# Kernel optimization log

Measured on AMD Instinct MI355X. Metric: run time of the kernel, lower is better.

Reference implementation:

```python
import jax, jax.numpy as jnp
import numpy as np

B, T, C, N = 4, 12, 64, 10000
H = 64            # d_inner (GRU hidden)
L = 2             # num_layers
NE = 2000         # number of static hyperedges
NNZ = 80000       # incidence list length
TOPK = 10         # HGCNADP_topk
DE = 16           # HGCNADP_embed_dims
RATE = 0.5        # hyperedge_rate (blend static vs adaptive)


def setup_inputs() -> dict:
    key = jax.random.key(0)
    ks = jax.random.split(key, 10)
    scale = 0.05
    x = jax.random.normal(ks[0], (B, T, C, N), jnp.float32)
    node_idx = jax.random.randint(ks[1], (NNZ,), 0, N, jnp.int32)
    edge_idx = jax.random.randint(ks[2], (NNZ,), 0, NE, jnp.int32)
    hyperedge_index = jnp.stack([node_idx, edge_idx])  # (2, NNZ)
    node_embs = jax.random.normal(ks[3], (L, N, DE), jnp.float32) * 0.1
    W_zr = jax.random.normal(ks[4], (L, C + H, 2 * H), jnp.float32) * scale
    b_zr = jnp.zeros((L, 2 * H), jnp.float32)
    W_c = jax.random.normal(ks[5], (L, C + H, H), jnp.float32) * scale
    b_c = jnp.zeros((L, H), jnp.float32)
    W_out = jax.random.normal(ks[6], (L, H, C), jnp.float32) * scale
    b_out = jnp.zeros((L, C), jnp.float32)
    return {"x": x, "hyperedge_index": hyperedge_index, "node_embs": node_embs,
            "W_zr": W_zr, "b_zr": b_zr, "W_c": W_c, "b_c": b_c,
            "W_out": W_out, "b_out": b_out}


def reference(x, hyperedge_index, node_embs, W_zr, b_zr, W_c, b_c, W_out, b_out):
    # x: (B, T, C, N). Dropout is identity (eval mode).
    node_idx = hyperedge_index[0]
    edge_idx = hyperedge_index[1]
    edge_deg = jnp.zeros((NE,), x.dtype).at[edge_idx].add(1.0)
    inv_e = 1.0 / jnp.maximum(edge_deg, 1.0)
    node_deg = jnp.zeros((N,), x.dtype).at[node_idx].add(1.0)
    inv_n = 1.0 / jnp.maximum(node_deg, 1.0)

    def conv(f, topk_idx, topk_w):
        # f: (B, N, D). Static hypergraph pass: node -> hyperedge -> node.
        msg = jnp.take(f, node_idx, axis=1)                       # (B, NNZ, D)
        eagg = jnp.zeros((f.shape[0], NE, f.shape[2]), f.dtype).at[:, edge_idx].add(msg)
        eagg = eagg * inv_e[None, :, None]                        # (B, NE, D)
        stat = jnp.zeros_like(f).at[:, node_idx].add(jnp.take(eagg, edge_idx, axis=1))
        stat = stat * inv_n[None, :, None]                        # (B, N, D)
        # Adaptive top-k hyperedge aggregation (softmax-weighted neighbor sum).
        adp = jnp.einsum('bnkd,nk->bnd', jnp.take(f, topk_idx, axis=1), topk_w)
        return RATE * stat + (1.0 - RATE) * adp

    out = x
    for l in range(L):
        xl = out.transpose(0, 1, 3, 2)                            # (B, T, N, C)
        E = node_embs[l]
        scores = jax.nn.relu(E @ E.T)                             # (N, N)
        vals, idx = jax.lax.top_k(scores, TOPK)                   # (N, K)
        w = jax.nn.softmax(vals, axis=-1)
        Wz, bz = W_zr[l], b_zr[l]
        Wc_, bc_ = W_c[l], b_c[l]
        Wo, bo = W_out[l], b_out[l]

        def step(h, x_t):
            zr = jax.nn.sigmoid(conv(jnp.concatenate([x_t, h], -1), idx, w) @ Wz + bz)
            z, r = jnp.split(zr, 2, axis=-1)
            c = jnp.tanh(conv(jnp.concatenate([x_t, r * h], -1), idx, w) @ Wc_ + bc_)
            h_new = z * h + (1.0 - z) * c
            return h_new, h_new @ Wo + bo

        h0 = jnp.zeros((out.shape[0], N, H), x.dtype)
        _, ys = jax.lax.scan(step, h0, xl.transpose(1, 0, 2, 3))  # ys: (T, B, N, C)
        out = out + ys.transpose(1, 0, 3, 2)                      # residual, back to (B,T,C,N)
    return out
```

## Files before the change

### kernel.cpp

```cpp
#include <hip/hip_runtime.h>
#include <hip/hip_fp16.h>
#include <cstdio>

#define BB 4
#define TT 12
#define CC 64
#define NN 10000
#define HH 64
#define LL 2
#define NEDGE 2000
#define NNZT 80000
#define KTOP 10
#define DEMB 16
#define BT (BB*TT)
#define TOPK_BLKS 1250
#define TRN_BLKS 30048
#define NB16 625

typedef long long ll;
typedef unsigned long long u64;
typedef unsigned int u32;
typedef unsigned short ushort;

typedef short bf16x8 __attribute__((ext_vector_type(8)));
typedef float f32x4 __attribute__((ext_vector_type(4)));

__device__ __forceinline__ void up8(const uint4 v, float* f) {
  const __half2* p = reinterpret_cast<const __half2*>(&v);
  float2 t0 = __half22float2(p[0]);
  float2 t1 = __half22float2(p[1]);
  float2 t2 = __half22float2(p[2]);
  float2 t3 = __half22float2(p[3]);
  f[0]=t0.x; f[1]=t0.y; f[2]=t1.x; f[3]=t1.y;
  f[4]=t2.x; f[5]=t2.y; f[6]=t3.x; f[7]=t3.y;
}
__device__ __forceinline__ uint4 pk8(const float* f) {
  __half2 h0 = __floats2half2_rn(f[0], f[1]);
  __half2 h1 = __floats2half2_rn(f[2], f[3]);
  __half2 h2 = __floats2half2_rn(f[4], f[5]);
  __half2 h3 = __floats2half2_rn(f[6], f[7]);
  uint4 r;
  r.x = *reinterpret_cast<unsigned*>(&h0);
  r.y = *reinterpret_cast<unsigned*>(&h1);
  r.z = *reinterpret_cast<unsigned*>(&h2);
  r.w = *reinterpret_cast<unsigned*>(&h3);
  return r;
}
__device__ __forceinline__ ushort f2bf(float x) {
  u32 u = __float_as_uint(x);
  u32 r = u + 0x7FFFu + ((u >> 16) & 1u);
  return (ushort)(r >> 16);
}
__device__ __forceinline__ uint4 pk8bf(const float* f) {
  uint4 r;
  r.x = (u32)f2bf(f[0]) | ((u32)f2bf(f[1])<<16);
  r.y = (u32)f2bf(f[2]) | ((u32)f2bf(f[3])<<16);
  r.z = (u32)f2bf(f[4]) | ((u32)f2bf(f[5])<<16);
  r.w = (u32)f2bf(f[6]) | ((u32)f2bf(f[7])<<16);
  return r;
}

__global__ void deg_kernel(const int* __restrict__ nidx, const int* __restrict__ eidx,
                           int* __restrict__ ndeg, int* __restrict__ edeg) {
  int i = blockIdx.x*256 + threadIdx.x;
  if (i < NNZT) { atomicAdd(&ndeg[nidx[i]],1); atomicAdd(&edeg[eidx[i]],1); }
}

__global__ void exscan_kernel(const int* __restrict__ cnt, int* __restrict__ off, int n) {
  __shared__ int part[256];
  int tid = threadIdx.x;
  int chunk = (n + 255)/256;
  int lo = tid*chunk, hi = min(lo+chunk, n);
  int s = 0;
  for (int i=lo; i<hi; ++i) s += cnt[i];
  part[tid]=s; __syncthreads();
  if (tid==0){ int acc=0; for(int i=0;i<256;++i){int v=part[i];part[i]=acc;acc+=v;} off[n]=acc; }
  __syncthreads();
  int acc = part[tid];
  for (int i=lo; i<hi; ++i){ off[i]=acc; acc+=cnt[i]; }
}

__global__ void fill_csr_kernel(const int* __restrict__ nidx, const int* __restrict__ eidx,
                                const int* __restrict__ noff, const int* __restrict__ eoff,
                                int* __restrict__ ncur, int* __restrict__ ecur,
                                int* __restrict__ node_edges, int* __restrict__ edge_nodes) {
  int i = blockIdx.x*256 + threadIdx.x;
  if (i >= NNZT) return;
  int n = nidx[i], e = eidx[i];
  int pn = atomicAdd(&ncur[n],1);
  node_edges[noff[n]+pn] = e;
  int pe = atomicAdd(&ecur[e],1);
  edge_nodes[eoff[e]+pe] = n;
}

__global__ void invdeg_kernel(const int* __restrict__ ndeg, const int* __restrict__ edeg,
                              float* __restrict__ inv_n, float* __restrict__ inv_e) {
  int i = blockIdx.x*256+threadIdx.x;
  if (i < NN) inv_n[i] = 1.0f/fmaxf((float)ndeg[i],1.0f);
  if (i < NEDGE) inv_e[i] = 1.0f/fmaxf((float)edeg[i],1.0f);
}

__global__ void prep_w_kernel(const float* __restrict__ W_zr, const float* __restrict__ W_c,
                              const float* __restrict__ W_o,
                              short* __restrict__ Wz_swb, short* __restrict__ Wc_swb,
                              short* __restrict__ Wo_swb) {
  int l = blockIdx.y;
  const float* Wz = W_zr + (size_t)l*128*128;
  const float* Wc = W_c  + (size_t)l*128*64;
  const float* Wo = W_o  + (size_t)l*64*64;
  short* Wz_sw = Wz_swb + (size_t)l*16384;
  short* Wc_sw = Wc_swb + (size_t)l*8192;
  short* Wo_sw = Wo_swb + (size_t)l*4096;
  int idx = blockIdx.x*256 + threadIdx.x;
  if (idx < 16384) {
    int i = idx&7, lane = (idx>>3)&63, kk = (idx>>9)&3, tc = idx>>11;
    int k = kk*32 + (lane>>4)*8 + i, col = tc*16 + (lane&15);
    Wz_sw[idx] = (short)f2bf(Wz[k*128+col]);
  }
  if (idx < 8192) {
    int i = idx&7, lane = (idx>>3)&63, kk = (idx>>9)&3, tc = idx>>11;
    int k = kk*32 + (lane>>4)*8 + i, col = tc*16 + (lane&15);
    Wc_sw[idx] = (short)f2bf(Wc[k*64+col]);
  }
  if (idx < 4096) {
    int i = idx&7, lane = (idx>>3)&63, kk = (idx>>9)&1, tc = idx>>10;
    int k = kk*32 + (lane>>4)*8 + i, col = tc*16 + (lane&15);
    Wo_sw[idx] = (short)f2bf(Wo[k*64+col]);
  }
}

__device__ __forceinline__ u64 sortstep(u64 X, int j, bool dir, int lane) {
  u64 p = __shfl_xor(X, j);
  bool lower = ((lane & j) == 0);
  bool keep_min = (dir == lower);
  bool xlt = (X < p);
  u64 mn = xlt ? X : p;
  u64 mx = xlt ? p : X;
  return keep_min ? mn : mx;
}

__device__ __forceinline__ void reselect(u64* bq, u64& thr, int& cnt, int lane) {
  int tot = 10 + cnt;
  u64 A = (lane < tot)      ? bq[lane]      : 0ull;
  u64 B = (lane + 64 < tot) ? bq[lane + 64] : 0ull;
  for (int k = 2; k <= 32; k <<= 1) {
    for (int j = k >> 1; j >= 1; j >>= 1) {
      bool dir = ((lane & k) == 0);
      A = sortstep(A, j, dir, lane);
      B = sortstep(B, j, dir, lane);
    }
  }
  for (int j = 32; j >= 1; j >>= 1) {
    A = sortstep(A, j, true,  lane);
    B = sortstep(B, j, false, lane);
  }
  {
    bool lt = (A < B);
    u64 mn = lt ? A : B, mx = lt ? B : A;
    A = mn; B = mx;
  }
  for (int j = 32; j >= 1; j >>= 1) {
    A = sortstep(A, j, true, lane);
    B = sortstep(B, j, true, lane);
  }
  if (lane >= 54) bq[63 - lane] = B;
  thr = __shfl(B, 54);
  cnt = 0;
}

__device__ void topk_body(int layer, int qb, char* smem,
                          const float* __restrict__ embs, int2* __restrict__ tkc_b) {
  u64 (*buf)[128] = (u64(*)[128])smem;
  const float* E = embs + (ll)layer*NN*DEMB;
  int2* tkc = tkc_b + (ll)layer*NN*KTOP;
  int tid = threadIdx.x;
  int wv = tid >> 6, lane = tid & 63;
  int qbase = qb*16 + wv*4;
  const float4* E4 = (const float4*)E;
  float4 q[4][4];
  #pragma unroll
  for (int u=0;u<4;++u) {
    int n = qbase + u;
    #pragma unroll
    for (int j=0;j<4;++j) q[u][j] = E4[(ll)n*4 + j];
  }
  u64 thr[4] = {0,0,0,0};
  float thrf[4] = {0.f,0.f,0.f,0.f};
  int cnt[4] = {0,0,0,0};
  buf[tid>>4][tid&15] = 0ull;
  float4 a0,a1,a2,a3;
  {
    int ca = (lane < NN) ? lane : 0;
    a0=E4[(ll)ca*4]; a1=E4[(ll)ca*4+1]; a2=E4[(ll)ca*4+2]; a3=E4[(ll)ca*4+3];
  }
  for (int cb=0; cb<NN; cb+=64) {
    float4 b0,b1,b2,b3;
    int ncb = cb + 64;
    if (ncb < NN) {
      int cand2 = ncb + lane;
      int ca2 = (cand2 < NN) ? cand2 : 0;
      b0=E4[(ll)ca2*4]; b1=E4[(ll)ca2*4+1]; b2=E4[(ll)ca2*4+2]; b3=E4[(ll)ca2*4+3];
    }
    int cand = cb + lane;
    bool valid = (cand < NN);
    u64 low = (u64)(0x00FFFFFFu - (unsigned)cand);
    float sv[4];
    #pragma unroll
    for (int u=0;u<4;++u) {
      float dot = q[u][0].x*a0.x + q[u][0].y*a0.y + q[u][0].z*a0.z + q[u][0].w*a0.w
                + q[u][1].x*a1.x + q[u][1].y*a1.y + q[u][1].z*a1.z + q[u][1].w*a1.w
                + q[u][2].x*a2.x + q[u][2].y*a2.y + q[u][2].z*a2.z + q[u][2].w*a2.w
                + q[u][3].x*a3.x + q[u][3].y*a3.y + q[u][3].z*a3.z + q[u][3].w*a3.w;
      float s = fmaxf(dot, 0.f);
      sv[u] = valid ? s : -1.f;
    }
    bool hitany = (sv[0]>=thrf[0]) | (sv[1]>=thrf[1]) | (sv[2]>=thrf[2]) | (sv[3]>=thrf[3]);
    u64 anym = __ballot(hitany);
    if (anym) {
      #pragma unroll
      for (int u=0;u<4;++u) {
        u64 mask = __ballot(sv[u] >= thrf[u]);
        if (mask) {
          if (sv[u] >= thrf[u]) {
            u64 key = ((u64)__float_as_uint(sv[u]) << 32) | low;
            int myofs = (int)__popcll(mask & ((1ull<<lane)-1ull));
            buf[wv*4+u][10 + cnt[u] + myofs] = key;
          }
          cnt[u] += (int)__popcll(mask);
          if (cnt[u] >= 40) {
            reselect(&buf[wv*4+u][0], thr[u], cnt[u], lane);
            thrf[u] = __uint_as_float((u32)(thr[u] >> 32));
          }
        }
      }
    }
    a0=b0; a1=b1; a2=b2; a3=b3;
  }
  #pragma unroll
  for (int u=0;u<4;++u) {
    u64* bq = &buf[wv*4+u][0];
    if (cnt[u] > 0) reselect(bq, thr[u], cnt[u], lane);
    u64 k10 = (lane < 10) ? bq[lane] : 0ull;
    float v = __uint_as_float((unsigned)(k10 >> 32));
    int idx = 0x00FFFFFF - (int)(k10 & 0xFFFFFFFFull);
    float v0 = __shfl(v, 0);
    float e = (lane < 10) ? expf(v - v0) : 0.f;
    float s = e;
    for (int o=1;o<16;o<<=1) s += __shfl_xor(s, o);
    if (lane < 10) {
      int n = qbase + u;
      tkc[n*KTOP + lane] = make_int2(idx, __float_as_int(e / s));
    }
  }
}

__device__ void transpose_body(int tb, char* smem,
                               const float* __restrict__ src, __half* __restrict__ dst) {
  float (*tile)[33] = (float(*)[33])smem;
  int tid = threadIdx.x;
  int tx = tid & 31, ty = tid >> 5;
  int bt = tb / 626;
  int rem = tb % 626;
  int n0 = (rem % 313)*32, c0 = (rem/313)*32;
  for (int i=ty; i<32; i+=8) {
    int c = c0+i, nn = n0+tx;
    tile[i][tx] = (nn<NN)? src[((ll)bt*CC + c)*NN + nn] : 0.0f;
  }
  __syncthreads();
  for (int i=ty; i<32; i+=8) {
    int nn = n0+i, c = c0+tx;
    if (nn<NN) dst[((ll)bt*NN+nn)*64 + c] = __float2half_rn(tile[tx][i]);
  }
}

__global__ void __launch_bounds__(256) mega1_kernel(const float* __restrict__ embs,
                                                    int2* __restrict__ tkc,
                                                    const float* __restrict__ x,
                                                    __half* __restrict__ xt) {
  __shared__ __align__(16) char smem[16384];
  int bid = blockIdx.x;
  if (bid < TOPK_BLKS) topk_body(bid/625, bid%625, smem, embs, tkc);
  else transpose_body(bid - TOPK_BLKS, smem, x, xt);
}

__global__ void __launch_bounds__(256) edge_agg_kernel(
    const uint4* __restrict__ f8, uint4* __restrict__ eagg8,
    const int* __restrict__ eoff, const int* __restrict__ enodes,
    const float* __restrict__ inv_e) {
  __shared__ int en_s[1088];
  __shared__ int jo_s[17];
  int tid = threadIdx.x;
  int e0 = blockIdx.x*16;
  int s = blockIdx.y;
  if (tid < 17) jo_s[tid] = eoff[e0 + tid];
  __syncthreads();
  int jb0 = jo_s[0], cnt = jo_s[16] - jb0;
  bool stg = (cnt <= 1088);
  if (stg) for (int i = tid; i < cnt; i += 256) en_s[i] = enodes[jb0 + i];
  __syncthreads();
  int esub = tid>>4;
  int e = e0 + esub;
  int hsel = (tid>>3)&1;
  int lane8 = tid&7;
  int j0 = jo_s[esub] - jb0, j1 = jo_s[esub+1] - jb0;
  const uint4* fb = f8 + (ll)s*NN*8;
  float acc[8] = {0,0,0,0,0,0,0,0};
  for (int j = j0 + hsel; j < j1; j += 2) {
    int node = stg ? en_s[j] : enodes[jb0+j];
    float t[8]; up8(fb[(ll)node*8 + lane8], t);
    #pragma unroll
    for (int q=0;q<8;++q) acc[q] += t[q];
  }
  #pragma unroll
  for (int q=0;q<8;++q) acc[q] += __shfl_xor(acc[q], 8);
  if (hsel == 0) {
    float sc = inv_e[e];
    #pragma unroll
    for (int q=0;q<8;++q) acc[q] *= sc;
    eagg8[((ll)s*NEDGE+e)*8 + lane8] = pk8(acc);
  }
}

__global__ void __launch_bounds__(256) edge_agg8_kernel(
    const uint4* __restrict__ f8, uint4* __restrict__ eagg8,
    const int* __restrict__ eoff, const int* __restrict__ enodes,
    const float* __restrict__ inv_e) {
  __shared__ int en_s[576];
  __shared__ int jo_s[9];
  int tid = threadIdx.x;
  int e0 = blockIdx.x*8;
  int s = blockIdx.y;
  if (tid < 9) jo_s[tid] = eoff[e0 + tid];
  __syncthreads();
  int jb0 = jo_s[0], cnt = jo_s[8] - jb0;
  bool stg = (cnt <= 576);
  if (stg) for (int i = tid; i < cnt; i += 256) en_s[i] = enodes[jb0 + i];
  __syncthreads();
  int esub = tid>>5;
  int e = e0 + esub;
  int sub = (tid>>3)&3;
  int lane8 = tid&7;
  int j0 = jo_s[esub] - jb0, j1 = jo_s[esub+1] - jb0;
  const uint4* fb = f8 + (ll)s*NN*8;
  float acc[8] = {0,0,0,0,0,0,0,0};
  for (int j = j0 + sub; j < j1; j += 4) {
    int node = stg ? en_s[j] : enodes[jb0+j];
    float t[8]; up8(fb[(ll)node*8 + lane8], t);
    #pragma unroll
    for (int q=0;q<8;++q) acc[q] += t[q];
  }
  #pragma unroll
  for (int q=0;q<8;++q) acc[q] += __shfl_xor(acc[q], 8);
  #pragma unroll
  for (int q=0;q<8;++q) acc[q] += __shfl_xor(acc[q], 16);
  if (sub == 0) {
    float sc = inv_e[e];
    #pragma unroll
    for (int q=0;q<8;++q) acc[q] *= sc;
    eagg8[((ll)s*NEDGE+e)*8 + lane8] = pk8(acc);
  }
}

__global__ void __launch_bounds__(256) conv_x_kernel(
    const uint4* __restrict__ xt8, const uint4* __restrict__ eagg8,
    const int* __restrict__ noff, const int* __restrict__ nedges,
    const float* __restrict__ inv_n,
    const int2* __restrict__ tkc,
    uint4* __restrict__ cx8) {
  __shared__ int tki_s[32][KTOP];
  __shared__ float tkw_s[32][KTOP];
  __shared__ int ne_s[640];
  __shared__ int no_s[33];
  int tid = threadIdx.x; int s = blockIdx.y; int n0 = blockIdx.x*32;
  if (tid < 33) no_s[tid] = noff[min(n0 + tid, NN)];
  for (int i=tid; i<32*KTOP; i+=256) {
    int r=i/KTOP, k=i%KTOP; int n = n0+r;
    int2 p = (n<NN)? tkc[n*KTOP+k] : make_int2(0,0);
    tki_s[r][k] = p.x;
    tkw_s[r][k] = __int_as_float(p.y);
  }
  __syncthreads();
  int jb0 = no_s[0], cnt = no_s[32] - jb0;
  bool stg = (cnt <= 640);
  if (stg) for (int i=tid; i<cnt; i+=256) ne_s[i] = nedges[jb0+i];
  __syncthreads();
  int row = tid>>3, lane8 = tid&7;
  int n = n0 + row;
  if (n >= NN) return;
  float stv[8] = {0,0,0,0,0,0,0,0};
  const uint4* eb = eagg8 + (ll)s*NEDGE*8;
  int j0 = no_s[row] - jb0, j1 = no_s[row+1] - jb0;
  for (int j=j0;j<j1;++j) {
    int eidx = stg ? ne_s[j] : nedges[jb0+j];
    float t[8]; up8(eb[(ll)eidx*8 + lane8], t);
    #pragma unroll
    for (int q=0;q<8;++q) stv[q] += t[q];
  }
  float sc = 0.5f*inv_n[n];
  float adv[8] = {0,0,0,0,0,0,0,0};
  const uint4* xb = xt8 + (ll)s*NN*8;
  #pragma unroll
  for (int k=0;k<KTOP;++k) {
    float w = tkw_s[row][k];
    float t[8]; up8(xb[(ll)tki_s[row][k]*8 + lane8], t);
    #pragma unroll
    for (int q=0;q<8;++q) adv[q] += w*t[q];
  }
  float r8[8];
  #pragma unroll
  for (int q=0;q<8;++q) r8[q] = sc*stv[q] + 0.5f*adv[q];
  cx8[((ll)s*NN+n)*8+lane8] = pk8bf(r8);
}

__global__ void __launch_bounds__(256) step0_kernel(
    const uint4* __restrict__ cx8,
    const short* __restrict__ Wz_sw, const float* __restrict__ bz,
    const short* __restrict__ Wc_sw, const float* __restrict__ bc,
    const short* __restrict__ Wo_sw, const float* __restrict__ bo,
    __half* __restrict__ h, float* __restrict__ out, __half* __restrict__ xtn) {
  __shared__ __align__(16) short in_bf[16][72];
  __shared__ __align__(16) short hn[16][72];
  __shared__ __align__(16) float yt[64][20];
  __shared__ __align__(16) __half hwsh[16][64];
  __shared__ __align__(16) float ot[16][68];
  int tid = threadIdx.x;
  int b = blockIdx.y; int n0 = blockIdx.x*16;
  int bt = b*TT;
  if (tid < 128) {
    int row = tid>>3, lane8 = tid&7;
    int n = n0 + row;
    *(uint4*)&in_bf[row][lane8*8] = cx8[((ll)bt*NN + n)*8 + lane8];
  }
  __syncthreads();
  int wv = tid>>6, lane = tid&63;
  int m = lane&15, g = lane>>4;
  {
    int tc = wv;
    f32x4 az = {0.f,0.f,0.f,0.f};
    f32x4 ac = {0.f,0.f,0.f,0.f};
    #pragma unroll
    for (int kk=0;kk<2;++kk) {
      bf16x8 a = *(const bf16x8*)&in_bf[m][kk*32 + g*8];
      bf16x8 bwz = *(const bf16x8*)&Wz_sw[((tc*4+kk)*64 + lane)*8];
      bf16x8 bwc = *(const bf16x8*)&Wc_sw[((tc*4+kk)*64 + lane)*8];
      az = __builtin_amdgcn_mfma_f32_16x16x32_bf16(a, bwz, az, 0, 0, 0);
      ac = __builtin_amdgcn_mfma_f32_16x16x32_bf16(a, bwc, ac, 0, 0, 0);
    }
    int col = tc*16 + m;
    float bzv = bz[col], bcv = bc[col];
    #pragma unroll
    for (int r=0;r<4;++r) {
      int row = g*4 + r;
      float z = 1.0f/(1.0f+expf(-(az[r]+bzv)));
      float cval = tanhf(ac[r]+bcv);
      float hnew = (1.0f-z)*cval;
      hwsh[row][col] = __float2half_rn(hnew);
      hn[row][col] = (short)f2bf(hnew);
    }
  }
  __syncthreads();
  {
    int tc = wv;
    f32x4 acc = {0.f,0.f,0.f,0.f};
    #pragma unroll
    for (int kk=0;kk<2;++kk) {
      bf16x8 a = *(const bf16x8*)&hn[m][kk*32 + g*8];
      bf16x8 bw = *(const bf16x8*)&Wo_sw[((tc*2+kk)*64 + lane)*8];
      acc = __builtin_amdgcn_mfma_f32_16x16x32_bf16(a, bw, acc, 0, 0, 0);
    }
    int col = tc*16 + m;
    float bias = bo[col];
    #pragma unroll
    for (int r=0;r<4;++r) yt[col][g*4 + r] = acc[r] + bias;
  }
  __syncthreads();
  {
    int col = tid>>2, q = tid&3;
    int n = n0 + q*4;
    float4 y = *(const float4*)&yt[col][q*4];
    float4* dst = (float4*)&out[((ll)bt*64+col)*NN + n];
    float4 cur = *dst;
    cur.x += y.x; cur.y += y.y; cur.z += y.z; cur.w += y.w;
    *dst = cur;
    ot[q*4+0][col] = cur.x;
    ot[q*4+1][col] = cur.y;
    ot[q*4+2][col] = cur.z;
    ot[q*4+3][col] = cur.w;
  }
  __syncthreads();
  if (tid < 128) {
    int row = tid>>3, lane8 = tid&7;
    int n = n0 + row;
    ((uint4*)h)[((ll)b*NN+n)*8 + lane8] = *(uint4*)&hwsh[row][lane8*8];
    if (xtn) ((uint4*)xtn)[((ll)bt*NN+n)*8 + lane8] = pk8(&ot[row][lane8*8]);
  }
}

__global__ void __launch_bounds__(256) step_zr_kernel(
    const uint4* __restrict__ h8, const uint4* __restrict__ cx8,
    const uint4* __restrict__ eagg8,
    const short* __restrict__ Wz_sw, const float* __restrict__ bz,
    const int* __restrict__ noff, const int* __restrict__ nedges,
    const float* __restrict__ inv_n,
    const int2* __restrict__ tkc,
    __half* __restrict__ rh, __half* __restrict__ zout, int t) {
  __shared__ __align__(16) short in_bf[16][136];
  __shared__ __align__(16) __half zsh[16][64];
  __shared__ __align__(16) __half rsh[16][64];
  __shared__ __align__(16) __half hsh[16][64];
  __shared__ int tki_s[16][KTOP];
  __shared__ float tkw_s[16][KTOP];
  __shared__ int ne_s[384];
  __shared__ int no_s[17];
  int tid = threadIdx.x;
  int b = blockIdx.y; int n0 = blockIdx.x*16;
  int bt = b*TT + t;
  if (tid < 17) no_s[tid] = noff[n0 + tid];
  for (int i=tid; i<16*KTOP; i+=256) {
    int r=i/KTOP, k=i%KTOP;
    int2 p = tkc[(n0+r)*KTOP+k];
    tki_s[r][k] = p.x;
    tkw_s[r][k] = __int_as_float(p.y);
  }
  __syncthreads();
  int jb0 = no_s[0], ecnt = no_s[16] - jb0;
  bool stg = (ecnt <= 384);
  if (stg) for (int i=tid; i<ecnt; i+=256) ne_s[i] = nedges[jb0+i];
  __syncthreads();
  if (tid < 128) {
    int row = tid>>3, lane8 = tid&7;
    int n = n0 + row;
    uint4 cxv4 = cx8[((ll)bt*NN + n)*8 + lane8];
    *(uint4*)&hsh[row][lane8*8] = h8[((ll)b*NN+n)*8 + lane8];
    float stv[8] = {0,0,0,0,0,0,0,0};
    int j0 = no_s[row] - jb0, j1 = no_s[row+1] - jb0;
    const uint4* eb = eagg8 + (ll)b*NEDGE*8;
    for (int j=j0;j<j1;++j) {
      int eidx = stg ? ne_s[j] : nedges[jb0+j];
      float t8[8]; up8(eb[(ll)eidx*8 + lane8], t8);
      #pragma unroll
      for (int q=0;q<8;++q) stv[q] += t8[q];
    }
    float sc = 0.5f*inv_n[n];
    const uint4* hb = h8 + (ll)b*NN*8;
    float adv[8] = {0,0,0,0,0,0,0,0};
    #pragma unroll
    for (int k=0;k<KTOP;++k) {
      float w = tkw_s[row][k];
      float t8[8]; up8(hb[(ll)tki_s[row][k]*8 + lane8], t8);
      #pragma unroll
      for (int q=0;q<8;++q) adv[q] += w*t8[q];
    }
    float chv[8];
    #pragma unroll
    for (int q=0;q<8;++q) chv[q] = sc*stv[q] + 0.5f*adv[q];
    *(uint4*)&in_bf[row][lane8*8]    = cxv4;
    *(uint4*)&in_bf[row][64+lane8*8] = pk8bf(chv);
  }
  __syncthreads();
  int wv = tid>>6, lane = tid&63;
  int m = lane&15, g = lane>>4;
  #pragma unroll
  for (int q=0;q<2;++q) {
    int tc = wv + 4*q;
    f32x4 acc = {0.f,0.f,0.f,0.f};
    #pragma unroll
    for (int kk=0;kk<4;++kk) {
      bf16x8 a = *(const bf16x8*)&in_bf[m][kk*32 + g*8];
      bf16x8 bf = *(const bf16x8*)&Wz_sw[((tc*4+kk)*64 + lane)*8];
      acc = __builtin_amdgcn_mfma_f32_16x16x32_bf16(a, bf, acc, 0, 0, 0);
    }
    int col = tc*16 + m;
    float bias = bz[col];
    #pragma unroll
    for (int r=0;r<4;++r) {
      int row = g*4 + r;
      float v = 1.0f/(1.0f+expf(-(acc[r]+bias)));
      if (col < 64) zsh[row][col] = __float2half_rn(v);
      else {
        int c = col-64;
        float hv = __half2float(hsh[row][c]);
        rsh[row][c] = __float2half_rn(v*hv);
      }
    }
  }
  __syncthreads();
  {
    int row = (tid&127)>>3, lane8 = tid&7;
    int n = n0 + row;
    if (tid < 128) ((uint4*)zout)[((ll)b*NN+n)*8 + lane8] = *(uint4*)&zsh[row][lane8*8];
    else           ((uint4*)rh)[((ll)b*NN+n)*8 + lane8]   = *(uint4*)&rsh[row][lane8*8];
  }
}

__global__ void __launch_bounds__(256) step_hy_kernel(
    const uint4* __restrict__ rh8, const uint4* __restrict__ cx8,
    const uint4* __restrict__ eagg8,
    const short* __restrict__ Wc_sw, const float* __restrict__ bc,
    const short* __restrict__ Wo_sw, const float* __restrict__ bo,
    const int* __restrict__ noff, const int* __restrict__ nedges,
    const float* __restrict__ inv_n,
    const int2* __restrict__ tkc,
    const __half* __restrict__ zbuf, __half* __restrict__ h,
    float* __restrict__ out, __half* __restrict__ xtn, int t) {
  __shared__ __align__(16) short in_bf[16][136];
  __shared__ __align__(16) short hn[16][72];
  __shared__ __align__(16) float yt[64][20];
  __shared__ __align__(16) __half zsh[16][64];
  __shared__ __align__(16) __half hosh[16][64];
  __shared__ __align__(16) __half hwsh[16][64];
  __shared__ __align__(16) float ot[16][68];
  __shared__ int tki_s[16][KTOP];
  __shared__ float tkw_s[16][KTOP];
  __shared__ int ne_s[384];
  __shared__ int no_s[17];
  int tid = threadIdx.x;
  int b = blockIdx.y; int n0 = blockIdx.x*16;
  int bt = b*TT + t;
  if (tid < 17) no_s[tid] = noff[n0 + tid];
  for (int i=tid; i<16*KTOP; i+=256) {
    int r=i/KTOP, k=i%KTOP;
    int2 p = tkc[(n0+r)*KTOP+k];
    tki_s[r][k] = p.x;
    tkw_s[r][k] = __int_as_float(p.y);
  }
  __syncthreads();
  int jb0 = no_s[0], ecnt = no_s[16] - jb0;
  bool stg = (ecnt <= 384);
  if (stg) for (int i=tid; i<ecnt; i+=256) ne_s[i] = nedges[jb0+i];
  __syncthreads();
  if (tid < 128) {
    int row = tid>>3, lane8 = tid&7;
    int n = n0 + row;
    uint4 cxv4 = cx8[((ll)bt*NN + n)*8 + lane8];
    *(uint4*)&zsh[row][lane8*8]  = ((const uint4*)zbuf)[((ll)b*NN+n)*8 + lane8];
    *(uint4*)&hosh[row][lane8*8] = ((const uint4*)h)[((ll)b*NN+n)*8 + lane8];
    float stv[8] = {0,0,0,0,0,0,0,0};
    int j0 = no_s[row] - jb0, j1 = no_s[row+1] - jb0;
    const uint4* eb = eagg8 + (ll)b*NEDGE*8;
    for (int j=j0;j<j1;++j) {
      int eidx = stg ? ne_s[j] : nedges[jb0+j];
      float t8[8]; up8(eb[(ll)eidx*8 + lane8], t8);
      #pragma unroll
      for (int q=0;q<8;++q) stv[q] += t8[q];
    }
    float sc = 0.5f*inv_n[n];
    const uint4* rb = rh8 + (ll)b*NN*8;
    float adv[8] = {0,0,0,0,0,0,0,0};
    #pragma unroll
    for (int k=0;k<KTOP;++k) {
      float w = tkw_s[row][k];
      float t8[8]; up8(rb[(ll)tki_s[row][k]*8 + lane8], t8);
      #pragma unroll
      for (int q=0;q<8;++q) adv[q] += w*t8[q];
    }
    float chv[8];
    #pragma unroll
    for (int q=0;q<8;++q) chv[q] = sc*stv[q] + 0.5f*adv[q];
    *(uint4*)&in_bf[row][lane8*8]    = cxv4;
    *(uint4*)&in_bf[row][64+lane8*8] = pk8bf(chv);
  }
  __syncthreads();
  int wv = tid>>6, lane = tid&63;
  int m = lane&15, g = lane>>4;
  {
    int tc = wv;
    f32x4 acc = {0.f,0.f,0.f,0.f};
    #pragma unroll
    for (int kk=0;kk<4;++kk) {
      bf16x8 a = *(const bf16x8*)&in_bf[m][kk*32 + g*8];
      bf16x8 bf = *(const bf16x8*)&Wc_sw[((tc*4+kk)*64 + lane)*8];
      acc = __builtin_amdgcn_mfma_f32_16x16x32_bf16(a, bf, acc, 0, 0, 0);
    }
    int col = tc*16 + m;
    float bias = bc[col];
    #pragma unroll
    for (int r=0;r<4;++r) {
      int row = g*4 + r;
      float cval = tanhf(acc[r]+bias);
      float z = __half2float(zsh[row][col]);
      float hv = __half2float(hosh[row][col]);
      float hnew = z*hv + (1.0f-z)*cval;
      hwsh[row][col] = __float2half_rn(hnew);
      hn[row][col] = (short)f2bf(hnew);
    }
  }
  __syncthreads();
  {
    int tc = wv;
    f32x4 acc = {0.f,0.f,0.f,0.f};
    #pragma unroll
    for (int kk=0;kk<2;++kk) {
      bf16x8 a = *(const bf16x8*)&hn[m][kk*32 + g*8];
      bf16x8 bf = *(const bf16x8*)&Wo_sw[((tc*2+kk)*64 + lane)*8];
      acc = __builtin_amdgcn_mfma_f32_16x16x32_bf16(a, bf, acc, 0, 0, 0);
    }
    int col = tc*16 + m;
    float bias = bo[col];
    #pragma unroll
    for (int r=0;r<4;++r) yt[col][g*4 + r] = acc[r] + bias;
  }
  __syncthreads();
  {
    int col = tid>>2, q = tid&3;
    int n = n0 + q*4;
    float4 y = *(const float4*)&yt[col][q*4];
    float4* dst = (float4*)&out[((ll)bt*64+col)*NN + n];
    float4 cur = *dst;
    cur.x += y.x; cur.y += y.y; cur.z += y.z; cur.w += y.w;
    *dst = cur;
    ot[q*4+0][col] = cur.x;
    ot[q*4+1][col] = cur.y;
    ot[q*4+2][col] = cur.z;
    ot[q*4+3][col] = cur.w;
  }
  __syncthreads();
  if (tid < 128) {
    int row = tid>>3, lane8 = tid&7;
    int n = n0 + row;
    ((uint4*)h)[((ll)b*NN+n)*8 + lane8] = *(uint4*)&hwsh[row][lane8*8];
    if (xtn) ((uint4*)xtn)[((ll)bt*NN+n)*8 + lane8] = pk8(&ot[row][lane8*8]);
  }
}

extern "C" void kernel_launch(void* const* d_in, const int* in_sizes, int n_in,
                              void* d_out, int out_size, void* d_ws, size_t ws_size,
                              hipStream_t stream) {
  const float* x    = (const float*)d_in[0];
  const int*  hidx  = (const int*)d_in[1];
  const float* embs = (const float*)d_in[2];
  const float* W_zr = (const float*)d_in[3];
  const float* b_zr = (const float*)d_in[4];
  const float* W_c  = (const float*)d_in[5];
  const float* b_c  = (const float*)d_in[6];
  const float* W_out= (const float*)d_in[7];
  const float* b_out= (const float*)d_in[8];
  const int* node_idx = hidx;
  const int* edge_idx = hidx + NNZT;

  char* ws = (char*)d_ws;
  size_t off = 0;
  auto alloc = [&](size_t bytes) -> void* {
    void* p = ws + off; off += (bytes + 255) & ~(size_t)255; return p;
  };
  __half* xt    = (__half*)alloc((size_t)BT*NN*64*2);
  __half* cx    = (__half*)alloc((size_t)BT*NN*64*2);
  __half* eaggx = (__half*)alloc((size_t)BT*NEDGE*64*2);
  __half* eaggh = (__half*)alloc((size_t)BB*NEDGE*64*2);
  __half* hbuf  = (__half*)alloc((size_t)BB*NN*64*2);
  __half* rhbuf = (__half*)alloc((size_t)BB*NN*64*2);
  __half* zbuf  = (__half*)alloc((size_t)BB*NN*64*2);
  short* Wz_sw = (short*)alloc((size_t)LL*16384*2);
  short* Wc_sw = (short*)alloc((size_t)LL*8192*2);
  short* Wo_sw = (short*)alloc((size_t)LL*4096*2);
  int2* tkc    = (int2*)alloc((size_t)LL*NN*KTOP*8);
  float* inv_e = (float*)alloc(NEDGE*4);
  float* inv_n = (float*)alloc(NN*4);
  int* ndeg    = (int*)alloc(NN*4);
  int* edeg    = (int*)alloc(NEDGE*4);
  int* noff    = (int*)alloc((NN+1)*4);
  int* eoff    = (int*)alloc((NEDGE+1)*4);
  int* ncur    = (int*)alloc(NN*4);
  int* ecur    = (int*)alloc(NEDGE*4);
  int* nedges  = (int*)alloc(NNZT*4);
  int* enodes  = (int*)alloc(NNZT*4);
  if (off > ws_size) {
    fprintf(stderr, "kernel_launch: ws too small, need %zu have %zu\n", off, ws_size);
    return;
  }

  hipMemcpyAsync(d_out, x, (size_t)BB*TT*CC*NN*4, hipMemcpyDeviceToDevice, stream);

  hipMemsetAsync(ndeg, 0, NN*4, stream);
  hipMemsetAsync(edeg, 0, NEDGE*4, stream);
  hipMemsetAsync(ncur, 0, NN*4, stream);
  hipMemsetAsync(ecur, 0, NEDGE*4, stream);
  deg_kernel<<<(NNZT+255)/256,256,0,stream>>>(node_idx, edge_idx, ndeg, edeg);
  exscan_kernel<<<1,256,0,stream>>>(ndeg, noff, NN);
  exscan_kernel<<<1,256,0,stream>>>(edeg, eoff, NEDGE);
  fill_csr_kernel<<<(NNZT+255)/256,256,0,stream>>>(node_idx, edge_idx, noff, eoff,
                                                   ncur, ecur, nedges, enodes);
  invdeg_kernel<<<(NN+255)/256,256,0,stream>>>(ndeg, edeg, inv_n, inv_e);

  prep_w_kernel<<<dim3(64,LL),256,0,stream>>>(W_zr, W_c, W_out, Wz_sw, Wc_sw, Wo_sw);
  float* outp = (float*)d_out;
  mega1_kernel<<<TOPK_BLKS + TRN_BLKS,256,0,stream>>>(embs, tkc, outp, xt);

  for (int l=0; l<LL; ++l) {
    const short* Wzs = Wz_sw + (size_t)l*16384;
    const short* Wcs = Wc_sw + (size_t)l*8192;
    const short* Wos = Wo_sw + (size_t)l*4096;
    const float* bz = b_zr + l*128;
    const float* bc = b_c + l*64;
    const float* bo = b_out + l*64;
    const int2* tkcl = tkc + (size_t)l*NN*KTOP;
    __half* xtn = (l < LL-1) ? xt : (__half*)nullptr;
    edge_agg_kernel<<<dim3(125, BT),256,0,stream>>>(
        (const uint4*)xt, (uint4*)eaggx, eoff, enodes, inv_e);
    conv_x_kernel<<<dim3(313, BT),256,0,stream>>>(
        (const uint4*)xt, (const uint4*)eaggx, noff, nedges, inv_n, tkcl, (uint4*)cx);
    step0_kernel<<<dim3(NB16, BB),256,0,stream>>>(
        (const uint4*)cx, Wzs, bz, Wcs, bc, Wos, bo, hbuf, outp, xtn);
    for (int t=1; t<TT; ++t) {
      edge_agg8_kernel<<<dim3(250, BB),256,0,stream>>>(
          (const uint4*)hbuf, (uint4*)eaggh, eoff, enodes, inv_e);
      step_zr_kernel<<<dim3(NB16, BB),256,0,stream>>>(
          (const uint4*)hbuf, (const uint4*)cx, (const uint4*)eaggh, Wzs, bz,
          noff, nedges, inv_n, tkcl, rhbuf, zbuf, t);
      edge_agg8_kernel<<<dim3(250, BB),256,0,stream>>>(
          (const uint4*)rhbuf, (uint4*)eaggh, eoff, enodes, inv_e);
      step_hy_kernel<<<dim3(NB16, BB),256,0,stream>>>(
          (const uint4*)rhbuf, (const uint4*)cx, (const uint4*)eaggh, Wcs, bc, Wos, bo,
          noff, nedges, inv_n, tkcl, zbuf, hbuf, outp, xtn, t);
    }
  }
}
```

Measured before the change: 2.230 ms.

## Screen top-k candidates with bf16 MFMA scores and recompute exact fp32 for hits

The top-k scoring loop now computes approximate E·E^T scores with bf16 MFMA instructions on a bf16 copy of the embeddings, made by a new conversion kernel. Only candidates whose approximate score clears the current threshold minus a small epsilon are rescored exactly in fp32 and inserted into the selection buffer. This moves the dominant N×N dot-product work from scalar FMAs onto matrix cores. In exchange it adds a conversion kernel, scattered fp32 reloads for hits, and a correctness risk if bf16 error ever exceeds the epsilon margin.

New measurement: 2.771 ms. +24.3%, slower.

```diff
diff --git a/kernel.cpp b/kernel.cpp
--- a/kernel.cpp
+++ b/kernel.cpp
@@ -16,6 +16,7 @@
 #define TOPK_BLKS 1250
 #define TRN_BLKS 30048
 #define NB16 625
+#define EPS_TK 0.01f
 
 typedef long long ll;
 typedef unsigned long long u64;
@@ -129,6 +130,12 @@
   }
 }
 
+__global__ void ebf_kernel(const float* __restrict__ embs, ushort* __restrict__ Ebf) {
+  int l = blockIdx.y;
+  int i = blockIdx.x*256 + threadIdx.x;
+  if (i < NN*DEMB) Ebf[(ll)l*NN*DEMB + i] = f2bf(embs[(ll)l*NN*DEMB + i]);
+}
+
 __device__ __forceinline__ u64 sortstep(u64 X, int j, bool dir, int lane) {
   u64 p = __shfl_xor(X, j);
   bool lower = ((lane & j) == 0);
@@ -169,77 +176,96 @@
 }
 
 __device__ void topk_body(int layer, int qb, char* smem,
-                          const float* __restrict__ embs, int2* __restrict__ tkc_b) {
+                          const float* __restrict__ embs,
+                          const ushort* __restrict__ Ebf_all,
+                          int2* __restrict__ tkc_b) {
   u64 (*buf)[128] = (u64(*)[128])smem;
   const float* E = embs + (ll)layer*NN*DEMB;
+  const ushort* Ebf = Ebf_all + (ll)layer*NN*DEMB;
   int2* tkc = tkc_b + (ll)layer*NN*KTOP;
   int tid = threadIdx.x;
   int wv = tid >> 6, lane = tid & 63;
+  int m = lane & 15, g = lane >> 4;
   int qbase = qb*16 + wv*4;
   const float4* E4 = (const float4*)E;
-  float4 q[4][4];
-  #pragma unroll
-  for (int u=0;u<4;++u) {
-    int n = qbase + u;
-    #pragma unroll
-    for (int j=0;j<4;++j) q[u][j] = E4[(ll)n*4 + j];
-  }
+  bf16x8 a_frag = {0,0,0,0,0,0,0,0};
+  if (m < 4 && g < 2) a_frag = *(const bf16x8*)&Ebf[(ll)(qbase + m)*DEMB + g*8];
   u64 thr[4] = {0,0,0,0};
-  float thrf[4] = {0.f,0.f,0.f,0.f};
+  float tf[4] = {-1.f,-1.f,-1.f,-1.f};
+  float smin = -1.f;
   int cnt[4] = {0,0,0,0};
   buf[tid>>4][tid&15] = 0ull;
-  float4 a0,a1,a2,a3;
-  {
-    int ca = (lane < NN) ? lane : 0;
-    a0=E4[(ll)ca*4]; a1=E4[(ll)ca*4+1]; a2=E4[(ll)ca*4+2]; a3=E4[(ll)ca*4+3];
-  }
-  for (int cb=0; cb<NN; cb+=64) {
-    float4 b0,b1,b2,b3;
-    int ncb = cb + 64;
-    if (ncb < NN) {
-      int cand2 = ncb + lane;
-      int ca2 = (cand2 < NN) ? cand2 : 0;
-      b0=E4[(ll)ca2*4]; b1=E4[(ll)ca2*4+1]; b2=E4[(ll)ca2*4+2]; b3=E4[(ll)ca2*4+3];
-    }
-    int cand = cb + lane;
-    bool valid = (cand < NN);
-    u64 low = (u64)(0x00FFFFFFu - (unsigned)cand);
-    float sv[4];
-    #pragma unroll
-    for (int u=0;u<4;++u) {
-      float dot = q[u][0].x*a0.x + q[u][0].y*a0.y + q[u][0].z*a0.z + q[u][0].w*a0.w
-                + q[u][1].x*a1.x + q[u][1].y*a1.y + q[u][1].z*a1.z + q[u][1].w*a1.w
-                + q[u][2].x*a2.x + q[u][2].y*a2.y + q[u][2].z*a2.z + q[u][2].w*a2.w
-                + q[u][3].x*a3.x + q[u][3].y*a3.y + q[u][3].z*a3.z + q[u][3].w*a3.w;
-      float s = fmaxf(dot, 0.f);
-      sv[u] = valid ? s : -1.f;
-    }
-    bool hitany = (sv[0]>=thrf[0]) | (sv[1]>=thrf[1]) | (sv[2]>=thrf[2]) | (sv[3]>=thrf[3]);
-    u64 anym = __ballot(hitany);
-    if (anym) {
+  for (int ct=0; ct<157; ++ct) {
+    int cb = ct*64;
+    bf16x8 b0={0,0,0,0,0,0,0,0}, b1={0,0,0,0,0,0,0,0};
+    bf16x8 b2={0,0,0,0,0,0,0,0}, b3={0,0,0,0,0,0,0,0};
+    if (g < 2) {
+      int c0 = min(cb + m,      NN-1);
+      int c1 = min(cb + 16 + m, NN-1);
+      int c2 = min(cb + 32 + m, NN-1);
+      int c3 = min(cb + 48 + m, NN-1);
+      b0 = *(const bf16x8*)&Ebf[(ll)c0*DEMB + g*8];
+      b1 = *(const bf16x8*)&Ebf[(ll)c1*DEMB + g*8];
+      b2 = *(const bf16x8*)&Ebf[(ll)c2*DEMB + g*8];
+      b3 = *(const bf16x8*)&Ebf[(ll)c3*DEMB + g*8];
+    }
+    f32x4 z4 = {0.f,0.f,0.f,0.f};
+    f32x4 acc0 = __builtin_amdgcn_mfma_f32_16x16x32_bf16(a_frag, b0, z4, 0, 0, 0);
+    f32x4 acc1 = __builtin_amdgcn_mfma_f32_16x16x32_bf16(a_frag, b1, z4, 0, 0, 0);
+    f32x4 acc2 = __builtin_amdgcn_mfma_f32_16x16x32_bf16(a_frag, b2, z4, 0, 0, 0);
+    f32x4 acc3 = __builtin_amdgcn_mfma_f32_16x16x32_bf16(a_frag, b3, z4, 0, 0, 0);
+    float mx0 = fmaxf(fmaxf(fmaxf(acc0[0],acc0[1]), fmaxf(acc0[2],acc0[3])), 0.f);
+    float mx1 = fmaxf(fmaxf(fmaxf(acc1[0],acc1[1]), fmaxf(acc1[2],acc1[3])), 0.f);
+    float mx2 = fmaxf(fmaxf(fmaxf(acc2[0],acc2[1]), fmaxf(acc2[2],acc2[3])), 0.f);
+    float mx3 = fmaxf(fmaxf(fmaxf(acc3[0],acc3[1]), fmaxf(acc3[2],acc3[3])), 0.f);
+    bool any = (g==0) && ((mx0>=smin) | (mx1>=smin) | (mx2>=smin) | (mx3>=smin));
+    if (__ballot(any)) {
+      int cbm = cb + m;
       #pragma unroll
-      for (int u=0;u<4;++u) {
-        u64 mask = __ballot(sv[u] >= thrf[u]);
-        if (mask) {
-          if (sv[u] >= thrf[u]) {
-            u64 key = ((u64)__float_as_uint(sv[u]) << 32) | low;
-            int myofs = (int)__popcll(mask & ((1ull<<lane)-1ull));
-            buf[wv*4+u][10 + cnt[u] + myofs] = key;
-          }
-          cnt[u] += (int)__popcll(mask);
-          if (cnt[u] >= 40) {
-            reselect(&buf[wv*4+u][0], thr[u], cnt[u], lane);
-            thrf[u] = __uint_as_float((u32)(thr[u] >> 32));
+      for (int r=0;r<4;++r) {
+        float s0 = fmaxf(acc0[r],0.f), s1 = fmaxf(acc1[r],0.f);
+        float s2 = fmaxf(acc2[r],0.f), s3 = fmaxf(acc3[r],0.f);
+        bool h0 = (g==0) && (cbm      < NN) && (s0 >= tf[r]);
+        bool h1 = (g==0) && (cbm+16   < NN) && (s1 >= tf[r]);
+        bool h2 = (g==0) && (cbm+32   < NN) && (s2 >= tf[r]);
+        bool h3 = (g==0) && (cbm+48   < NN) && (s3 >= tf[r]);
+        if (!__ballot(h0|h1|h2|h3)) continue;
+        #pragma unroll
+        for (int j=0;j<4;++j) {
+          bool hj = (j==0)?h0:(j==1)?h1:(j==2)?h2:h3;
+          u64 mk = __ballot(hj);
+          if (mk) {
+            if (hj) {
+              int c = cb + j*16 + m;
+              float4 c0 = E4[(ll)c*4],   c1 = E4[(ll)c*4+1];
+              float4 c2 = E4[(ll)c*4+2], c3 = E4[(ll)c*4+3];
+              float4 q0 = E4[(ll)(qbase+r)*4],   q1 = E4[(ll)(qbase+r)*4+1];
+              float4 q2 = E4[(ll)(qbase+r)*4+2], q3 = E4[(ll)(qbase+r)*4+3];
+              float dot = q0.x*c0.x + q0.y*c0.y + q0.z*c0.z + q0.w*c0.w
+                        + q1.x*c1.x + q1.y*c1.y + q1.z*c1.z + q1.w*c1.w
+                        + q2.x*c2.x + q2.y*c2.y + q2.z*c2.z + q2.w*c2.w
+                        + q3.x*c3.x + q3.y*c3.y + q3.z*c3.z + q3.w*c3.w;
+              float sx = fmaxf(dot, 0.f);
+              u64 key = ((u64)__float_as_uint(sx) << 32)
+                      | (u64)(0x00FFFFFFu - (unsigned)c);
+              int ofs = (int)__popcll(mk & ((1ull<<lane)-1ull));
+              buf[wv*4+r][10 + cnt[r] + ofs] = key;
+            }
+            cnt[r] += (int)__popcll(mk);
+            if (cnt[r] >= 40) {
+              reselect(&buf[wv*4+r][0], thr[r], cnt[r], lane);
+              tf[r] = __uint_as_float((u32)(thr[r] >> 32)) - EPS_TK;
+            }
           }
         }
       }
-    }
-    a0=b0; a1=b1; a2=b2; a3=b3;
+      smin = fminf(fminf(tf[0],tf[1]), fminf(tf[2],tf[3]));
+    }
   }
   #pragma unroll
-  for (int u=0;u<4;++u) {
-    u64* bq = &buf[wv*4+u][0];
-    if (cnt[u] > 0) reselect(bq, thr[u], cnt[u], lane);
+  for (int r=0;r<4;++r) {
+    u64* bq = &buf[wv*4+r][0];
+    if (cnt[r] > 0) reselect(bq, thr[r], cnt[r], lane);
     u64 k10 = (lane < 10) ? bq[lane] : 0ull;
     float v = __uint_as_float((unsigned)(k10 >> 32));
     int idx = 0x00FFFFFF - (int)(k10 & 0xFFFFFFFFull);
@@ -248,7 +274,7 @@
     float s = e;
     for (int o=1;o<16;o<<=1) s += __shfl_xor(s, o);
     if (lane < 10) {
-      int n = qbase + u;
+      int n = qbase + r;
       tkc[n*KTOP + lane] = make_int2(idx, __float_as_int(e / s));
     }
   }
@@ -274,12 +300,13 @@
 }
 
 __global__ void __launch_bounds__(256) mega1_kernel(const float* __restrict__ embs,
+                                                    const ushort* __restrict__ Ebf,
                                                     int2* __restrict__ tkc,
                                                     const float* __restrict__ x,
                                                     __half* __restrict__ xt) {
   __shared__ __align__(16) char smem[16384];
   int bid = blockIdx.x;
-  if (bid < TOPK_BLKS) topk_body(bid/625, bid%625, smem, embs, tkc);
+  if (bid < TOPK_BLKS) topk_body(bid/625, bid%625, smem, embs, Ebf, tkc);
   else transpose_body(bid - TOPK_BLKS, smem, x, xt);
 }
 
@@ -753,6 +780,7 @@
   short* Wz_sw = (short*)alloc((size_t)LL*16384*2);
   short* Wc_sw = (short*)alloc((size_t)LL*8192*2);
   short* Wo_sw = (short*)alloc((size_t)LL*4096*2);
+  ushort* Ebf  = (ushort*)alloc((size_t)LL*NN*DEMB*2);
   int2* tkc    = (int2*)alloc((size_t)LL*NN*KTOP*8);
   float* inv_e = (float*)alloc(NEDGE*4);
   float* inv_n = (float*)alloc(NN*4);
@@ -783,8 +811,9 @@
   invdeg_kernel<<<(NN+255)/256,256,0,stream>>>(ndeg, edeg, inv_n, inv_e);
 
   prep_w_kernel<<<dim3(64,LL),256,0,stream>>>(W_zr, W_c, W_out, Wz_sw, Wc_sw, Wo_sw);
+  ebf_kernel<<<dim3((NN*DEMB+255)/256, LL),256,0,stream>>>(embs, Ebf);
   float* outp = (float*)d_out;
-  mega1_kernel<<<TOPK_BLKS + TRN_BLKS,256,0,stream>>>(embs, tkc, outp, xt);
+  mega1_kernel<<<TOPK_BLKS + TRN_BLKS,256,0,stream>>>(embs, Ebf, tkc, outp, xt);
 
   for (int l=0; l<LL; ++l) {
     const short* Wzs = Wz_sw + (size_t)l*16384;
```
